# Kernel tuning notes

Measured on AMD Instinct MI355X. Metric: run time of the kernel, lower is better.

## Reference

```python
import jax, jax.numpy as jnp
from jax import lax
import numpy as np

B, T, C = 4, 2048, 1024
H = 4                      # num_heads
D = C // H                 # head_dim
EPS_N = 1e-6               # normalizer eps in scan
EPS_GN = 1e-5              # GroupNorm eps (torch default)


def setup_inputs() -> dict:
    key = jax.random.key(0)
    ks = jax.random.split(key, 8)
    s = 0.02
    return {
        "x": jax.random.normal(ks[0], (B, T, C), jnp.float32),
        "conv_w": jax.random.normal(ks[1], (C, 1, 4), jnp.float32) * s,
        "conv_b": jax.random.normal(ks[2], (C,), jnp.float32) * s,
        "wx_w": jax.random.normal(ks[3], (4 * C, C), jnp.float32) * s,
        "wx_b": jax.random.normal(ks[4], (4 * C,), jnp.float32) * s,
        "gn_w": jnp.ones((C,), jnp.float32),
        "gn_b": jnp.zeros((C,), jnp.float32),
        "out_w": jax.random.normal(ks[5], (C, C), jnp.float32) * s,
        "out_b": jax.random.normal(ks[6], (C,), jnp.float32) * s,
    }


def _slstm_scan(i_g, f_g, z_g, o_g):
    # all inputs (B,T,H,D); scan over time
    def step(carry, g):
        c, n, m = carry
        i_t, f_t, z_t, o_t = g
        m_t = jnp.maximum(f_t + m, i_t)
        i_p = jnp.exp(i_t - m_t)
        f_p = jnp.exp(f_t + m - m_t)
        c_t = f_p * c + i_p * z_t
        n_t = f_p * n + i_p
        h_t = jax.nn.sigmoid(o_t) * (c_t / (n_t + EPS_N))
        return (c_t, n_t, m_t), h_t

    tfirst = lambda a: jnp.transpose(a, (1, 0, 2, 3))  # (T,B,H,D)
    init = (jnp.zeros((B, H, D), i_g.dtype),
            jnp.ones((B, H, D), i_g.dtype),
            jnp.zeros((B, H, D), i_g.dtype))
    _, h_seq = lax.scan(step, init, (tfirst(i_g), tfirst(f_g), tfirst(z_g), tfirst(o_g)))
    return jnp.transpose(h_seq, (1, 0, 2, 3))  # (B,T,H,D)


def reference(x, conv_w, conv_b, wx_w, wx_b, gn_w, gn_b, out_w, out_b):
    # causal depthwise conv (torch pad=3 both sides, sliced to first T == left pad 3)
    xc = jnp.transpose(x, (0, 2, 1))  # (B,C,T)
    xc = lax.conv_general_dilated(
        xc, conv_w, window_strides=(1,), padding=[(3, 0)],
        dimension_numbers=("NCH", "OIH", "NCH"), feature_group_count=C)
    xc = jax.nn.silu(xc + conv_b[None, :, None])
    xc = jnp.transpose(xc, (0, 2, 1))  # (B,T,C)

    gates = jnp.einsum("btc,gc->btg", xc, wx_w) + wx_b  # (B,T,4C)
    gates = gates.reshape(B, T, 4, H, D)
    i_g, f_g, z_g, o_g = (gates[:, :, k] for k in range(4))
    z_g = jnp.tanh(z_g)

    h = _slstm_scan(i_g, f_g, z_g, o_g).reshape(B, T, C)

    # GroupNorm(H groups) over (B,C,T): normalize per (batch, group) over (D, T)
    hg = h.reshape(B, T, H, D)
    mean = hg.mean(axis=(1, 3), keepdims=True)
    var = hg.var(axis=(1, 3), keepdims=True)
    hn = ((hg - mean) / jnp.sqrt(var + EPS_GN)).reshape(B, T, C)
    hn = hn * gn_w + gn_b

    out = jnp.einsum("btc,oc->bto", hn, out_w) + out_b
    return out + x  # dropout is identity at inference
```

## Files before the change

### kernel.cpp

```cpp
#include <hip/hip_runtime.h>

#define B_ 4
#define T_ 2048
#define C_ 1024
#define H_ 4
#define D_ 256
#define M_ (B_*T_)
#define N1_ (4*C_)
#define K_ C_
#define LANES_ (B_*C_)
#define CHUNK_ 32
#define NCHUNK_ (T_/CHUNK_)

typedef unsigned short u16;
typedef unsigned int u32;
typedef __bf16 bf16x8 __attribute__((ext_vector_type(8)));
typedef float f32x4 __attribute__((ext_vector_type(4)));
typedef float vf4 __attribute__((ext_vector_type(4)));
typedef unsigned short u16x4 __attribute__((ext_vector_type(4)));
typedef unsigned short u16x8 __attribute__((ext_vector_type(8)));

__device__ __forceinline__ u16 f2bf(float f) {
  union { float f; u32 u; } v; v.f = f;
  u32 u = v.u;
  u32 r = (u + 0x7FFFu + ((u >> 16) & 1u)) >> 16;
  return (u16)r;
}
__device__ __forceinline__ float b2f(u16 h) {
  union { u32 u; float f; } v; v.u = ((u32)h) << 16;
  return v.f;
}

__global__ void cast_weights(const float* __restrict__ wx_w, const float* __restrict__ out_w,
                             u16* __restrict__ w1p, u16* __restrict__ w2) {
  int i8 = (blockIdx.x * 256 + threadIdx.x) * 8;
  u16x8 o;
  if (i8 < N1_ * K_) {
    int n = i8 >> 10, k8 = i8 & 1023;
    const float* src = wx_w + (size_t)(((n & 3) << 10) | (n >> 2)) * K_ + k8;
    vf4 a = *(const vf4*)src;
    vf4 b = *(const vf4*)(src + 4);
#pragma unroll
    for (int j = 0; j < 4; ++j) { o[j] = f2bf(a[j]); o[j + 4] = f2bf(b[j]); }
    *(u16x8*)(w1p + i8) = o;
  } else {
    int j8 = i8 - N1_ * K_;
    vf4 a = *(const vf4*)(out_w + j8);
    vf4 b = *(const vf4*)(out_w + j8 + 4);
#pragma unroll
    for (int j = 0; j < 4; ++j) { o[j] = f2bf(a[j]); o[j + 4] = f2bf(b[j]); }
    *(u16x8*)(w2 + j8) = o;
  }
}

__global__ void conv_silu(const float* __restrict__ x, const float* __restrict__ cw,
                          const float* __restrict__ cb, u16* __restrict__ xc,
                          float* __restrict__ stats) {
  if (blockIdx.x == 0 && threadIdx.x < 32) stats[threadIdx.x] = 0.f;
  int i4 = (blockIdx.x * 256 + threadIdx.x) * 4;
  int c = i4 & (C_ - 1);
  int t = (i4 >> 10) & (T_ - 1);
  vf4 acc = *(const vf4*)(cb + c);
  vf4 w0 = *(const vf4*)(cw + (size_t)c * 4);
  vf4 w1 = *(const vf4*)(cw + (size_t)(c + 1) * 4);
  vf4 w2 = *(const vf4*)(cw + (size_t)(c + 2) * 4);
  vf4 w3 = *(const vf4*)(cw + (size_t)(c + 3) * 4);
#pragma unroll
  for (int k = 0; k < 4; ++k) {
    if (t - 3 + k >= 0) {
      vf4 xv = *(const vf4*)(x + (size_t)i4 + (size_t)(k - 3) * C_);
      acc[0] = fmaf(w0[k], xv[0], acc[0]);
      acc[1] = fmaf(w1[k], xv[1], acc[1]);
      acc[2] = fmaf(w2[k], xv[2], acc[2]);
      acc[3] = fmaf(w3[k], xv[3], acc[3]);
    }
  }
  u16x4 o;
#pragma unroll
  for (int j = 0; j < 4; ++j) {
    float s = acc[j] / (1.f + __expf(-acc[j]));
    o[j] = f2bf(s);
  }
  *(u16x4*)(xc + i4) = o;
}

template <int EPI>
__global__ __launch_bounds__(256, 2)
void gemm_bt(const u16* __restrict__ A, const u16* __restrict__ Bw,
             const float* __restrict__ bias, const float* __restrict__ resid,
             u16* __restrict__ obf, float* __restrict__ of32,
             f32x4* __restrict__ sSum, int M, int N, int K)
{
  __shared__ __align__(16) u16 smem[128 * 132];
  u16* a_s = smem;
  u16* b_s = smem + 128 * 64;

  const int tid  = threadIdx.x;
  const int lane = tid & 63;
  const int l15  = lane & 15;
  const int q    = lane >> 4;
  const int wave = tid >> 6;
  const int wm   = (wave >> 1) * 64;
  const int wn   = (wave & 1) * 64;
  const int bm   = blockIdx.y * 128;
  const int bn   = blockIdx.x * 128;

  const int srow   = wave * 8 + (lane >> 3);
  const int schunk = lane & 7;

  f32x4 acc[4][4];
#pragma unroll
  for (int i = 0; i < 4; ++i)
#pragma unroll
    for (int j = 0; j < 4; ++j) acc[i][j] = (f32x4){0.f, 0.f, 0.f, 0.f};

  for (int k0 = 0; k0 < K; k0 += 64) {
#pragma unroll
    for (int i = 0; i < 4; ++i) {
      int r = i * 32 + srow;
      int lc = schunk ^ (r & 7);
      const u16* ga = A  + (size_t)(bm + r) * K + k0 + lc * 8;
      const u16* gb = Bw + (size_t)(bn + r) * K + k0 + lc * 8;
      __builtin_amdgcn_global_load_lds(
          (const __attribute__((address_space(1))) u32*)ga,
          (__attribute__((address_space(3))) u32*)&a_s[(i * 32 + wave * 8) * 64],
          16, 0, 0);
      __builtin_amdgcn_global_load_lds(
          (const __attribute__((address_space(1))) u32*)gb,
          (__attribute__((address_space(3))) u32*)&b_s[(i * 32 + wave * 8) * 64],
          16, 0, 0);
    }
    __syncthreads();
#pragma unroll
    for (int kk = 0; kk < 64; kk += 32) {
      const int kc = kk >> 3;
      bf16x8 af[4], bfr[4];
#pragma unroll
      for (int s = 0; s < 4; ++s) {
        int ra = wm + s * 16 + l15;
        int ph = (kc + q) ^ (ra & 7);
        af[s] = *(const bf16x8*)&a_s[ra * 64 + ph * 8];
      }
#pragma unroll
      for (int s = 0; s < 4; ++s) {
        int rb = wn + s * 16 + l15;
        int ph = (kc + q) ^ (rb & 7);
        bfr[s] = *(const bf16x8*)&b_s[rb * 64 + ph * 8];
      }
#pragma unroll
      for (int sm = 0; sm < 4; ++sm)
#pragma unroll
        for (int sn = 0; sn < 4; ++sn)
          acc[sm][sn] = __builtin_amdgcn_mfma_f32_16x16x32_bf16(af[sm], bfr[sn], acc[sm][sn], 0, 0, 0);
    }
    __syncthreads();
  }

  if (EPI == 0) {
#pragma unroll
    for (int smi = 0; smi < 4; ++smi) {
#pragma unroll
      for (int r = 0; r < 4; ++r) {
        int lrow = wm + smi * 16 + q * 4 + r;
#pragma unroll
        for (int sni = 0; sni < 4; ++sni) {
          int lcol = wn + sni * 16 + l15;
          int gcol = bn + lcol;
          float v = acc[smi][sni][r] + bias[((gcol & 3) << 10) | (gcol >> 2)];
          if ((l15 & 3) == 2) {
            float e = __expf(2.f * v);
            v = (e - 1.f) / (e + 1.f);
          }
          u16 hv = f2bf(v);
          obf[(size_t)(bm + lrow) * N + gcol] = hv;
          smem[lrow * 132 + lcol] = hv;
        }
      }
    }
    __syncthreads();
    if (tid < 128) {
      int ch = tid & 31, ck = tid >> 5;
      const u16* sp = smem + (ck * 32) * 132 + ch * 4;
      float F = 0.f, Mx = -1e30f, aBc = 0.f, aBn = 0.f;
#pragma unroll 8
      for (int t = 0; t < CHUNK_; ++t) {
        u16x4 gv = *(const u16x4*)(sp + t * 132);
        float i_t = b2f(gv[0]), f_t = b2f(gv[1]), z_t = b2f(gv[2]);
        float Mf = Mx + f_t;
        float Mn = fmaxf(Mf, i_t);
        float ea = __expf(Mf - Mn), eb = __expf(i_t - Mn);
        aBc = ea * aBc + eb * z_t;
        aBn = ea * aBn + eb;
        F += f_t; Mx = Mn;
      }
      int b = bm >> 11;
      int s = ((bm & 2047) >> 5) + ck;
      int cg = (bn >> 2) + ch;
      sSum[(size_t)s * LANES_ + b * C_ + cg] = (f32x4){F, Mx, aBc, aBn};
    }
  } else {
#pragma unroll
    for (int smi = 0; smi < 4; ++smi) {
#pragma unroll
      for (int r = 0; r < 4; ++r) {
        int row = bm + wm + smi * 16 + q * 4 + r;
#pragma unroll
        for (int sni = 0; sni < 4; ++sni) {
          int col = bn + wn + sni * 16 + l15;
          float v = acc[smi][sni][r] + bias[col] + resid[(size_t)row * N + col];
          of32[(size_t)row * N + col] = v;
        }
      }
    }
  }
}

__global__ void scan_prefix(const f32x4* __restrict__ sSum, f32x4* __restrict__ iSt) {
  int l = blockIdx.x * 256 + threadIdx.x;
  float ct = 0.f, nt = 1.f, mt = 0.f;
#pragma unroll 4
  for (int s = 0; s < NCHUNK_; ++s) {
    int idx = s * LANES_ + l;
    f32x4 S = sSum[idx];
    iSt[idx] = (f32x4){ct, nt, mt, 0.f};
    float mf = mt + S[0];
    float mn = fmaxf(mf, S[1]);
    float a = __expf(mf - mn);
    float bcoef = __expf(S[1] - mn);
    ct = a * ct + bcoef * S[2];
    nt = a * nt + bcoef * S[3];
    mt = mn;
  }
}

__global__ void scan_passB(const u16* __restrict__ gates, const f32x4* __restrict__ iSt,
                           u16* __restrict__ h, float* __restrict__ stats) {
  int tid = blockIdx.x * 256 + threadIdx.x;
  int lp = tid & 2047;
  int s = tid >> 11;
  int b = lp >> 9;
  int c2 = (lp & 511) * 2;
  const u16* g = gates + ((size_t)(b * T_ + s * CHUNK_) * C_ + c2) * 4;
  u16* hp = h + (size_t)(b * T_ + s * CHUNK_) * C_ + c2;
  int idx = s * LANES_ + b * C_ + c2;
  f32x4 S0 = iSt[idx], S1 = iSt[idx + 1];
  float cc0 = S0[0], nn0 = S0[1], mm0 = S0[2];
  float cc1 = S1[0], nn1 = S1[1], mm1 = S1[2];
  float ls = 0.f, lq = 0.f;
#pragma unroll 4
  for (int t = 0; t < CHUNK_; ++t) {
    u16x8 gv = *(const u16x8*)(g + (size_t)t * C_ * 4);
    float h0, h1;
    {
      float i_t = b2f(gv[0]), f_t = b2f(gv[1]), z_t = b2f(gv[2]), o_t = b2f(gv[3]);
      float m_new = fmaxf(f_t + mm0, i_t);
      float i_p = __expf(i_t - m_new);
      float f_p = __expf(f_t + mm0 - m_new);
      cc0 = f_p * cc0 + i_p * z_t;
      nn0 = f_p * nn0 + i_p;
      mm0 = m_new;
      float sig_o = 1.f / (1.f + __expf(-o_t));
      h0 = sig_o * (cc0 / (nn0 + 1e-6f));
    }
    {
      float i_t = b2f(gv[4]), f_t = b2f(gv[5]), z_t = b2f(gv[6]), o_t = b2f(gv[7]);
      float m_new = fmaxf(f_t + mm1, i_t);
      float i_p = __expf(i_t - m_new);
      float f_p = __expf(f_t + mm1 - m_new);
      cc1 = f_p * cc1 + i_p * z_t;
      nn1 = f_p * nn1 + i_p;
      mm1 = m_new;
      float sig_o = 1.f / (1.f + __expf(-o_t));
      h1 = sig_o * (cc1 / (nn1 + 1e-6f));
    }
    u16 hb0 = f2bf(h0), hb1 = f2bf(h1);
    float v0 = b2f(hb0), v1 = b2f(hb1);
    ls += v0 + v1; lq += v0 * v0 + v1 * v1;
    *(u32*)(hp + (size_t)t * C_) = (u32)hb0 | ((u32)hb1 << 16);
  }
  __shared__ float rs[256], rq[256];
  int thr = threadIdx.x;
  rs[thr] = ls; rq[thr] = lq;
  __syncthreads();
  for (int off = 64; off > 0; off >>= 1) {
    if ((thr & 127) < off) { rs[thr] += rs[thr + off]; rq[thr] += rq[thr + off]; }
    __syncthreads();
  }
  if ((thr & 127) == 0) {
    int grp = b * 4 + (c2 >> 8);
    atomicAdd(&stats[grp * 2 + 0], rs[thr]);
    atomicAdd(&stats[grp * 2 + 1], rq[thr]);
  }
}

__global__ void norm_kernel(const u16* __restrict__ h, const float* __restrict__ stats,
                            const float* __restrict__ gn_w, const float* __restrict__ gn_b,
                            u16* __restrict__ hn) {
  int i8 = (blockIdx.x * 256 + threadIdx.x) * 8;
  int c = i8 & (C_ - 1);
  int b = i8 >> 21;
  int grp = b * 4 + (c >> 8);
  const float inv_n = 1.f / (float)(T_ * D_);
  float mean = stats[grp * 2 + 0] * inv_n;
  float var  = stats[grp * 2 + 1] * inv_n - mean * mean;
  float rstd = rsqrtf(var + 1e-5f);
  u16x8 hv = *(const u16x8*)(h + i8);
  vf4 w0 = *(const vf4*)(gn_w + c), w1 = *(const vf4*)(gn_w + c + 4);
  vf4 b0 = *(const vf4*)(gn_b + c), b1 = *(const vf4*)(gn_b + c + 4);
  u16x8 o;
#pragma unroll
  for (int j = 0; j < 4; ++j) {
    o[j]     = f2bf((b2f(hv[j])     - mean) * rstd * w0[j] + b0[j]);
    o[j + 4] = f2bf((b2f(hv[j + 4]) - mean) * rstd * w1[j] + b1[j]);
  }
  *(u16x8*)(hn + i8) = o;
}

extern "C" void kernel_launch(void* const* d_in, const int* in_sizes, int n_in,
                              void* d_out, int out_size, void* d_ws, size_t ws_size,
                              hipStream_t stream) {
  const float* x      = (const float*)d_in[0];
  const float* conv_w = (const float*)d_in[1];
  const float* conv_b = (const float*)d_in[2];
  const float* wx_w   = (const float*)d_in[3];
  const float* wx_b   = (const float*)d_in[4];
  const float* gn_w   = (const float*)d_in[5];
  const float* gn_b   = (const float*)d_in[6];
  const float* out_w  = (const float*)d_in[7];
  const float* out_b  = (const float*)d_in[8];
  float* out = (float*)d_out;

  char* p = (char*)d_ws;
  u16* xc    = (u16*)p; p += (size_t)M_ * K_ * 2;
  u16* w1    = (u16*)p; p += (size_t)N1_ * K_ * 2;
  u16* w2    = (u16*)p; p += (size_t)C_ * C_ * 2;
  u16* gts   = (u16*)p; p += (size_t)M_ * N1_ * 2;
  u16* hb    = (u16*)p; p += (size_t)M_ * C_ * 2;
  u16* hn    = (u16*)p; p += (size_t)M_ * C_ * 2;
  float* stats = (float*)p; p += 256;
  const int nsum = LANES_ * NCHUNK_;
  f32x4* sSum = (f32x4*)p; p += (size_t)nsum * 16;
  f32x4* iSt  = (f32x4*)p; p += (size_t)nsum * 16;

  cast_weights<<<(N1_ * K_ + C_ * C_) / 2048, 256, 0, stream>>>(wx_w, out_w, w1, w2);

  conv_silu<<<(M_ * C_) / 1024, 256, 0, stream>>>(x, conv_w, conv_b, xc, stats);

  gemm_bt<0><<<dim3(N1_ / 128, M_ / 128), 256, 0, stream>>>(
      xc, w1, wx_b, nullptr, gts, nullptr, sSum, M_, N1_, K_);

  scan_prefix<<<LANES_ / 256, 256, 0, stream>>>(sSum, iSt);
  scan_passB<<<(2048 * NCHUNK_) / 256, 256, 0, stream>>>(gts, iSt, hb, stats);

  norm_kernel<<<(M_ * C_) / 2048, 256, 0, stream>>>(hb, stats, gn_w, gn_b, hn);

  gemm_bt<1><<<dim3(C_ / 128, M_ / 128), 256, 0, stream>>>(
      hn, w2, out_b, x, nullptr, out, nullptr, M_, C_, K_);
}
```

Measured before the change: 282.3 us.

## Fuse prep kernels, stage GEMM epilogues through LDS for vectorized stores

Merges the weight-cast and conv+SiLU kernels into one launch to save a kernel launch. Both GEMM epilogues now stage results in shared memory and write them out as coalesced 16-byte vector stores; the second GEMM also reads the residual with vector loads. Bias values are hoisted into registers. Launch bounds rise to 3 blocks per CU, smem row padding changes from 132 to 136, and the scan_prefix unroll goes from 4 to 8. The epilogue staging adds extra barriers and LDS traffic, and the higher occupancy target may cause register spills.

```diff
diff --git a/kernel.cpp b/kernel.cpp
--- a/kernel.cpp
+++ b/kernel.cpp
@@ -31,39 +31,42 @@
   return v.f;
 }
 
-__global__ void cast_weights(const float* __restrict__ wx_w, const float* __restrict__ out_w,
-                             u16* __restrict__ w1p, u16* __restrict__ w2) {
-  int i8 = (blockIdx.x * 256 + threadIdx.x) * 8;
-  u16x8 o;
-  if (i8 < N1_ * K_) {
-    int n = i8 >> 10, k8 = i8 & 1023;
-    const float* src = wx_w + (size_t)(((n & 3) << 10) | (n >> 2)) * K_ + k8;
-    vf4 a = *(const vf4*)src;
-    vf4 b = *(const vf4*)(src + 4);
-#pragma unroll
-    for (int j = 0; j < 4; ++j) { o[j] = f2bf(a[j]); o[j + 4] = f2bf(b[j]); }
-    *(u16x8*)(w1p + i8) = o;
-  } else {
-    int j8 = i8 - N1_ * K_;
-    vf4 a = *(const vf4*)(out_w + j8);
-    vf4 b = *(const vf4*)(out_w + j8 + 4);
-#pragma unroll
-    for (int j = 0; j < 4; ++j) { o[j] = f2bf(a[j]); o[j + 4] = f2bf(b[j]); }
-    *(u16x8*)(w2 + j8) = o;
-  }
-}
-
-__global__ void conv_silu(const float* __restrict__ x, const float* __restrict__ cw,
-                          const float* __restrict__ cb, u16* __restrict__ xc,
-                          float* __restrict__ stats) {
-  if (blockIdx.x == 0 && threadIdx.x < 32) stats[threadIdx.x] = 0.f;
-  int i4 = (blockIdx.x * 256 + threadIdx.x) * 4;
+#define NCAST_ ((N1_*K_ + C_*C_) / 2048)
+
+__global__ void prep_kernel(const float* __restrict__ wx_w, const float* __restrict__ out_w,
+                            u16* __restrict__ w1p, u16* __restrict__ w2,
+                            const float* __restrict__ x, const float* __restrict__ cw,
+                            const float* __restrict__ cb, u16* __restrict__ xc,
+                            float* __restrict__ stats) {
+  if (blockIdx.x < NCAST_) {
+    int i8 = (blockIdx.x * 256 + threadIdx.x) * 8;
+    u16x8 o;
+    if (i8 < N1_ * K_) {
+      int n = i8 >> 10, k8 = i8 & 1023;
+      const float* src = wx_w + (size_t)(((n & 3) << 10) | (n >> 2)) * K_ + k8;
+      vf4 a = *(const vf4*)src;
+      vf4 b = *(const vf4*)(src + 4);
+#pragma unroll
+      for (int j = 0; j < 4; ++j) { o[j] = f2bf(a[j]); o[j + 4] = f2bf(b[j]); }
+      *(u16x8*)(w1p + i8) = o;
+    } else {
+      int j8 = i8 - N1_ * K_;
+      vf4 a = *(const vf4*)(out_w + j8);
+      vf4 b = *(const vf4*)(out_w + j8 + 4);
+#pragma unroll
+      for (int j = 0; j < 4; ++j) { o[j] = f2bf(a[j]); o[j + 4] = f2bf(b[j]); }
+      *(u16x8*)(w2 + j8) = o;
+    }
+    return;
+  }
+  if (blockIdx.x == NCAST_ && threadIdx.x < 32) stats[threadIdx.x] = 0.f;
+  int i4 = ((blockIdx.x - NCAST_) * 256 + threadIdx.x) * 4;
   int c = i4 & (C_ - 1);
   int t = (i4 >> 10) & (T_ - 1);
   vf4 acc = *(const vf4*)(cb + c);
   vf4 w0 = *(const vf4*)(cw + (size_t)c * 4);
   vf4 w1 = *(const vf4*)(cw + (size_t)(c + 1) * 4);
-  vf4 w2 = *(const vf4*)(cw + (size_t)(c + 2) * 4);
+  vf4 w2v = *(const vf4*)(cw + (size_t)(c + 2) * 4);
   vf4 w3 = *(const vf4*)(cw + (size_t)(c + 3) * 4);
 #pragma unroll
   for (int k = 0; k < 4; ++k) {
@@ -71,7 +74,7 @@
       vf4 xv = *(const vf4*)(x + (size_t)i4 + (size_t)(k - 3) * C_);
       acc[0] = fmaf(w0[k], xv[0], acc[0]);
       acc[1] = fmaf(w1[k], xv[1], acc[1]);
-      acc[2] = fmaf(w2[k], xv[2], acc[2]);
+      acc[2] = fmaf(w2v[k], xv[2], acc[2]);
       acc[3] = fmaf(w3[k], xv[3], acc[3]);
     }
   }
@@ -85,13 +88,13 @@
 }
 
 template <int EPI>
-__global__ __launch_bounds__(256, 2)
+__global__ __launch_bounds__(256, 3)
 void gemm_bt(const u16* __restrict__ A, const u16* __restrict__ Bw,
              const float* __restrict__ bias, const float* __restrict__ resid,
              u16* __restrict__ obf, float* __restrict__ of32,
              f32x4* __restrict__ sSum, int M, int N, int K)
 {
-  __shared__ __align__(16) u16 smem[128 * 132];
+  __shared__ __align__(16) u16 smem[128 * 136];
   u16* a_s = smem;
   u16* b_s = smem + 128 * 64;
 
@@ -107,6 +110,14 @@
 
   const int srow   = wave * 8 + (lane >> 3);
   const int schunk = lane & 7;
+
+  float bias4[4];
+#pragma unroll
+  for (int sn = 0; sn < 4; ++sn) {
+    int gcol = bn + wn + sn * 16 + l15;
+    bias4[sn] = (EPI == 0) ? bias[((gcol & 3) << 10) | (gcol >> 2)] : bias[gcol];
+  }
+  const bool zlane = (EPI == 0) && ((l15 & 3) == 2);
 
   f32x4 acc[4][4];
 #pragma unroll
@@ -165,26 +176,31 @@
 #pragma unroll
         for (int sni = 0; sni < 4; ++sni) {
           int lcol = wn + sni * 16 + l15;
-          int gcol = bn + lcol;
-          float v = acc[smi][sni][r] + bias[((gcol & 3) << 10) | (gcol >> 2)];
-          if ((l15 & 3) == 2) {
+          float v = acc[smi][sni][r] + bias4[sni];
+          if (zlane) {
             float e = __expf(2.f * v);
             v = (e - 1.f) / (e + 1.f);
           }
-          u16 hv = f2bf(v);
-          obf[(size_t)(bm + lrow) * N + gcol] = hv;
-          smem[lrow * 132 + lcol] = hv;
+          smem[lrow * 136 + lcol] = f2bf(v);
         }
       }
     }
     __syncthreads();
+#pragma unroll
+    for (int it = 0; it < 8; ++it) {
+      int flat = it * 256 + tid;
+      int row = flat >> 4;
+      int ch  = flat & 15;
+      u16x8 vv = *(const u16x8*)&smem[row * 136 + ch * 8];
+      *(u16x8*)(obf + (size_t)(bm + row) * N + bn + ch * 8) = vv;
+    }
     if (tid < 128) {
       int ch = tid & 31, ck = tid >> 5;
-      const u16* sp = smem + (ck * 32) * 132 + ch * 4;
+      const u16* sp = smem + (ck * 32) * 136 + ch * 4;
       float F = 0.f, Mx = -1e30f, aBc = 0.f, aBn = 0.f;
 #pragma unroll 8
       for (int t = 0; t < CHUNK_; ++t) {
-        u16x4 gv = *(const u16x4*)(sp + t * 132);
+        u16x4 gv = *(const u16x4*)(sp + t * 136);
         float i_t = b2f(gv[0]), f_t = b2f(gv[1]), z_t = b2f(gv[2]);
         float Mf = Mx + f_t;
         float Mn = fmaxf(Mf, i_t);
@@ -199,17 +215,34 @@
       sSum[(size_t)s * LANES_ + b * C_ + cg] = (f32x4){F, Mx, aBc, aBn};
     }
   } else {
-#pragma unroll
-    for (int smi = 0; smi < 4; ++smi) {
-#pragma unroll
-      for (int r = 0; r < 4; ++r) {
-        int row = bm + wm + smi * 16 + q * 4 + r;
-#pragma unroll
-        for (int sni = 0; sni < 4; ++sni) {
-          int col = bn + wn + sni * 16 + l15;
-          float v = acc[smi][sni][r] + bias[col] + resid[(size_t)row * N + col];
-          of32[(size_t)row * N + col] = v;
+    float* fs = (float*)smem;
+#pragma unroll
+    for (int h = 0; h < 2; ++h) {
+      __syncthreads();
+#pragma unroll
+      for (int smi2 = 0; smi2 < 2; ++smi2) {
+        int smi = 2 * h + smi2;
+#pragma unroll
+        for (int r = 0; r < 4; ++r) {
+          int slot = (wm >> 1) + smi2 * 16 + q * 4 + r;
+#pragma unroll
+          for (int sni = 0; sni < 4; ++sni) {
+            int lcol = wn + sni * 16 + l15;
+            fs[slot * 132 + lcol] = acc[smi][sni][r] + bias4[sni];
+          }
         }
+      }
+      __syncthreads();
+#pragma unroll
+      for (int it = 0; it < 8; ++it) {
+        int flat = it * 256 + tid;
+        int slot = flat >> 5;
+        int c4 = (flat & 31) * 4;
+        int absrow = bm + ((slot & 32) << 1) + (h << 5) + (slot & 31);
+        vf4 v = *(const vf4*)&fs[slot * 132 + c4];
+        vf4 rv = *(const vf4*)(resid + (size_t)absrow * N + bn + c4);
+        v[0] += rv[0]; v[1] += rv[1]; v[2] += rv[2]; v[3] += rv[3];
+        *(vf4*)(of32 + (size_t)absrow * N + bn + c4) = v;
       }
     }
   }
@@ -218,7 +251,7 @@
 __global__ void scan_prefix(const f32x4* __restrict__ sSum, f32x4* __restrict__ iSt) {
   int l = blockIdx.x * 256 + threadIdx.x;
   float ct = 0.f, nt = 1.f, mt = 0.f;
-#pragma unroll 4
+#pragma unroll 8
   for (int s = 0; s < NCHUNK_; ++s) {
     int idx = s * LANES_ + l;
     f32x4 S = sSum[idx];
@@ -342,9 +375,8 @@
   f32x4* sSum = (f32x4*)p; p += (size_t)nsum * 16;
   f32x4* iSt  = (f32x4*)p; p += (size_t)nsum * 16;
 
-  cast_weights<<<(N1_ * K_ + C_ * C_) / 2048, 256, 0, stream>>>(wx_w, out_w, w1, w2);
-
-  conv_silu<<<(M_ * C_) / 1024, 256, 0, stream>>>(x, conv_w, conv_b, xc, stats);
+  prep_kernel<<<NCAST_ + (M_ * C_) / 1024, 256, 0, stream>>>(
+      wx_w, out_w, w1, w2, x, conv_w, conv_b, xc, stats);
 
   gemm_bt<0><<<dim3(N1_ / 128, M_ / 128), 256, 0, stream>>>(
       xc, w1, wx_b, nullptr, gts, nullptr, sSum, M_, N1_, K_);
```

Result: faster. 273.9 us (-3.0%).
